# Performance work log

Hardware: AMD Instinct MI355X
Metric: run time of the kernel (lower is better)

The kernel has to match this reference:

```python
import jax, jax.numpy as jnp
import numpy as np
from jax import lax

EPS = 1e-5      # BatchNorm1d default eps
SLOPE = 0.01    # LeakyReLU default negative_slope
DN = ('NCDHW', 'OIDHW', 'NCDHW')
PAD_31 = ((1, 1), (0, 0), (1, 1))   # kernel (3,1,3), padding (1,0,1)
PAD_13 = ((0, 0), (1, 1), (1, 1))   # kernel (1,3,3), padding (0,1,1)
PAD_P = ((1, 1), (1, 1), (1, 1))    # pool kernel 3, padding 1
STRIDE_P = (2, 2, 1)                # height_pooling=False -> stride (2,2,1)


def setup_inputs() -> dict:
    key = jax.random.key(0)
    ks = jax.random.split(key, 8)
    B, Cin, Cout = 1, 32, 64
    D1, D2, D3 = 160, 160, 32
    mask = jax.random.randint(ks[0], (B, 1, D1, D2, D3), 0, 2) > 0
    x = jax.random.normal(ks[1], (B, Cin, D1, D2, D3), dtype=jnp.float32)

    def w(k, cin, cout, kd, kh, kw):
        return jax.random.normal(k, (cout, cin, kd, kh, kw), dtype=jnp.float32) * 0.05

    inp = {
        'x': x, 'mask': mask,
        'W_A1': w(ks[2], Cin, Cout, 3, 1, 3),
        'W_A2': w(ks[3], Cout, Cout, 1, 3, 3),
        'W_B1': w(ks[4], Cin, Cout, 1, 3, 3),
        'W_B2': w(ks[5], Cout, Cout, 3, 1, 3),
        'W_pool': w(ks[6], Cout, Cout, 3, 3, 3),
    }
    for name in ('A1', 'A2', 'B1', 'B2'):
        inp['g_' + name] = jnp.ones((Cout,), jnp.float32)
        inp['b_' + name] = jnp.zeros((Cout,), jnp.float32)
    return inp


def _conv(h, W, pad, stride=(1, 1, 1)):
    return lax.conv_general_dilated(h, W, stride, pad, dimension_numbers=DN)


def _lrelu(h):
    return jnp.where(h >= 0, h, SLOPE * h)


def _masked_bn(h, m, n_active, gamma, beta):
    # BatchNorm1d over the [N_active, C] sparse feature tensor:
    # per-channel stats over active voxels only (biased variance, training mode).
    mean = jnp.sum(h * m, axis=(0, 2, 3, 4)) / n_active
    mu = mean[None, :, None, None, None]
    var = jnp.sum(((h - mu) ** 2) * m, axis=(0, 2, 3, 4)) / n_active
    inv = lax.rsqrt(var + EPS)[None, :, None, None, None]
    out = (h - mu) * inv * gamma[None, :, None, None, None] + beta[None, :, None, None, None]
    return out * m  # keep inactive sites exactly zero


def reference(x, mask, W_A1, W_A2, W_B1, W_B2, W_pool,
              g_A1, b_A1, g_A2, b_A2, g_B1, b_B1, g_B2, b_B2):
    m = mask.astype(x.dtype)                      # [B,1,D1,D2,D3] active-site indicator
    n_active = jnp.sum(m)
    xs = x * m                                    # sparse input: zero at inactive voxels

    def subm(h, W, pad):
        # submanifold conv: compute only at active output sites (same site set as input)
        return _conv(h, W, pad) * m

    # branch A: conv3x1 -> LeakyReLU -> BN -> conv1x3 -> LeakyReLU -> BN
    res_A = _masked_bn(_lrelu(subm(xs, W_A1, PAD_31)), m, n_active, g_A1, b_A1)
    res_A = _masked_bn(_lrelu(subm(res_A, W_A2, PAD_13)), m, n_active, g_A2, b_A2)

    # branch B: conv1x3 -> LeakyReLU -> BN -> conv3x1 -> LeakyReLU -> BN
    res_B = _masked_bn(_lrelu(subm(xs, W_B1, PAD_13)), m, n_active, g_B1, b_B1)
    res_B = _masked_bn(_lrelu(subm(res_B, W_B2, PAD_31)), m, n_active, g_B2, b_B2)

    res_B = res_B + res_A

    # strided SparseConv3d pool: output active where any input in 3x3x3 window is active
    ones_k = jnp.ones((1, 1, 3, 3, 3), x.dtype)
    out_mask = (_conv(m, ones_k, PAD_P, STRIDE_P) > 0).astype(x.dtype)
    down = _conv(res_B, W_pool, PAD_P, STRIDE_P) * out_mask
    return (down, res_B)
```

## Files before the change

kernel.cpp:

```cpp
#include <hip/hip_runtime.h>

static constexpr int ND1=160, ND2=160, ND3=32;
static constexpr int SP  = ND1*ND2*ND3;
static constexpr int CO  = 64;
static constexpr int OD1=80, OD2=80, OD3=32;
static constexpr int OSP = OD1*OD2*OD3;
static constexpr int NSC = 64;

typedef __attribute__((ext_vector_type(8))) short  short8;
typedef __attribute__((ext_vector_type(4))) float  f32x4;

__device__ __forceinline__ float b2f(unsigned u){ return __uint_as_float(u<<16); }
__device__ __forceinline__ unsigned short f2b(float f){
    unsigned u = __float_as_uint(f);
    u += 0x7fffu + ((u>>16)&1u);
    return (unsigned short)(u>>16);
}

__global__ void k_detect(const unsigned char* __restrict__ mb, int* __restrict__ flag)
{
    __shared__ int lf;
    if (threadIdx.x == 0) lf = 0;
    __syncthreads();
    int f = 0;
    for (int i = blockIdx.x*256 + threadIdx.x; i < SP; i += gridDim.x*256) {
        unsigned char b = mb[i];
        if (b > 1) f |= 4;
        if (b != 0 && (i & 3)) f |= 1;
    }
    if (f) atomicOr(&lf, f);
    __syncthreads();
    if (threadIdx.x == 0 && lf) atomicOr(flag, lf);
}

__global__ void k_mask(const void* __restrict__ mraw, const int* __restrict__ flag,
                       float* __restrict__ m, float* __restrict__ nactN)
{
    int i = blockIdx.x*256 + threadIdx.x;
    int f = *flag;
    float v;
    if (f & 4)      v = (reinterpret_cast<const float*>(mraw)[i] != 0.f) ? 1.f : 0.f;
    else if (f & 1) v = (reinterpret_cast<const unsigned char*>(mraw)[i] != 0) ? 1.f : 0.f;
    else            v = (reinterpret_cast<const int*>(mraw)[i] != 0) ? 1.f : 0.f;
    m[i] = v;
    float s = v;
    #pragma unroll
    for (int off = 32; off > 0; off >>= 1) s += __shfl_xor(s, off);
    __shared__ float wsum[4];
    if ((threadIdx.x & 63) == 0) wsum[threadIdx.x >> 6] = s;
    __syncthreads();
    if (threadIdx.x == 0) atomicAdd(&nactN[blockIdx.x & (NSC-1)], wsum[0]+wsum[1]+wsum[2]+wsum[3]);
}

__global__ void k_finalize2(const float* __restrict__ SN0, const float* __restrict__ g0,
                            const float* __restrict__ b0, float* __restrict__ o0,
                            const float* __restrict__ SN1, const float* __restrict__ g1,
                            const float* __restrict__ b1, float* __restrict__ o1,
                            const float* __restrict__ nactN)
{
    const float* SN = blockIdx.x ? SN1 : SN0;
    const float* g  = blockIdx.x ? g1  : g0;
    const float* b  = blockIdx.x ? b1  : b0;
    float*       o  = blockIdx.x ? o1  : o0;
    int c = threadIdx.x;
    float s1 = 0.f, s2 = 0.f;
    #pragma unroll 4
    for (int k = 0; k < NSC; k++){
        s1 += SN[k*128 + c];
        s2 += SN[k*128 + 64 + c];
    }
    float nn = nactN[c];
    #pragma unroll
    for (int off = 32; off > 0; off >>= 1) nn += __shfl_xor(nn, off);
    float mean = s1 / nn;
    float var  = s2 / nn - mean*mean;
    float inv  = rsqrtf(var + 1e-5f);
    float sc   = inv * g[c];
    o[c]      = sc;
    o[64 + c] = b[c] - mean*sc;
}

__global__ void k_wprep_all(const float* __restrict__ WA1, const float* __restrict__ WA2,
                            const float* __restrict__ WB1, const float* __restrict__ WB2,
                            const float* __restrict__ WP,
                            unsigned short* __restrict__ tA1, unsigned short* __restrict__ tA2,
                            unsigned short* __restrict__ tB1, unsigned short* __restrict__ tB2,
                            unsigned short* __restrict__ tP)
{
    int i = blockIdx.x*256 + threadIdx.x;
    const float* W; unsigned short* Wt; int CIN, NT, base;
    if      (i < 18432)  { W=WA1; Wt=tA1; CIN=32; NT=9;  base=0; }
    else if (i < 55296)  { W=WA2; Wt=tA2; CIN=64; NT=9;  base=18432; }
    else if (i < 73728)  { W=WB1; Wt=tB1; CIN=32; NT=9;  base=55296; }
    else if (i < 110592) { W=WB2; Wt=tB2; CIN=64; NT=9;  base=73728; }
    else if (i < 221184) { W=WP;  Wt=tP;  CIN=64; NT=27; base=110592; }
    else return;
    int j = i - base;
    int ksub = j & 31;
    int t = j >> 5;
    int co = t & 63;
    int kc = t >> 6;
    int nch = CIN >> 5;
    int tap = kc / nch;
    int ci  = (kc - tap*nch)*32 + ksub;
    Wt[j] = f2b(W[((size_t)co*CIN + ci)*NT + tap]);
}

__global__ void k_prep_x(const float* __restrict__ x, const float* __restrict__ m,
                         unsigned short* __restrict__ xt, float* __restrict__ om)
{
    __shared__ float t[64][33];
    int sp0 = blockIdx.x*64;
    int tid = threadIdx.x;
    int c = tid>>6, s = tid&63;
    float mm = m[sp0+s];
    #pragma unroll
    for (int r=0;r<8;r++){
        int ci = c + r*4;
        t[s][ci] = x[(size_t)ci*SP + sp0 + s]*mm;
    }
    __syncthreads();
    int sp = tid>>2, c0 = (tid&3)*8;
    unsigned short o[8];
    #pragma unroll
    for (int i=0;i<8;i++) o[i] = f2b(t[sp][c0+i]);
    uint4 pk;
    pk.x = o[0] | ((unsigned)o[1]<<16);
    pk.y = o[2] | ((unsigned)o[3]<<16);
    pk.z = o[4] | ((unsigned)o[5]<<16);
    pk.w = o[6] | ((unsigned)o[7]<<16);
    *reinterpret_cast<uint4*>(xt + (size_t)(sp0+sp)*32 + c0) = pk;

    if (blockIdx.x < OSP/256){
        int i = blockIdx.x*256 + tid;
        int o3 = i & 31; int tt = i >> 5; int o2 = tt % OD2; int o1 = tt / OD2;
        float ssum = 0.f;
        for (int kd = 0; kd < 3; kd++) { int d1 = 2*o1 - 1 + kd; if ((unsigned)d1 >= ND1) continue;
          for (int kh = 0; kh < 3; kh++) { int d2 = 2*o2 - 1 + kh; if ((unsigned)d2 >= ND2) continue;
            for (int kw = 0; kw < 3; kw++) { int d3 = o3 - 1 + kw; if ((unsigned)d3 >= ND3) continue;
              ssum += m[(d1*ND2 + d2)*ND3 + d3];
            } } }
        om[i] = (ssum > 0.f) ? 1.f : 0.f;
    }
}

__global__ void k_resB(const unsigned short* __restrict__ hA, const unsigned short* __restrict__ hB,
                       const float* __restrict__ sA, const float* __restrict__ sB,
                       const float* __restrict__ m,
                       unsigned short* __restrict__ rbt, float* __restrict__ resf)
{
    __shared__ float t[64][65];
    __shared__ float ss[256];
    int tid = threadIdx.x;
    if (tid < 128){ ss[tid] = sA[tid]; ss[128+tid] = sB[tid]; }
    __syncthreads();
    int sp0 = blockIdx.x*64;
    int sp = tid>>2, c0 = (tid&3)*16;
    float mm = m[sp0+sp];
    const size_t base = (size_t)(sp0+sp)*64 + c0;
    uint4 a0 = *reinterpret_cast<const uint4*>(hA + base);
    uint4 a1 = *reinterpret_cast<const uint4*>(hA + base + 8);
    uint4 b0 = *reinterpret_cast<const uint4*>(hB + base);
    uint4 b1 = *reinterpret_cast<const uint4*>(hB + base + 8);
    unsigned ua[16] = {a0.x&0xffffu,a0.x>>16,a0.y&0xffffu,a0.y>>16,a0.z&0xffffu,a0.z>>16,a0.w&0xffffu,a0.w>>16,
                       a1.x&0xffffu,a1.x>>16,a1.y&0xffffu,a1.y>>16,a1.z&0xffffu,a1.z>>16,a1.w&0xffffu,a1.w>>16};
    unsigned ub[16] = {b0.x&0xffffu,b0.x>>16,b0.y&0xffffu,b0.y>>16,b0.z&0xffffu,b0.z>>16,b0.w&0xffffu,b0.w>>16,
                       b1.x&0xffffu,b1.x>>16,b1.y&0xffffu,b1.y>>16,b1.z&0xffffu,b1.z>>16,b1.w&0xffffu,b1.w>>16};
    unsigned short o[16];
    #pragma unroll
    for (int q=0;q<16;q++){
        int ci = c0+q;
        float v = (b2f(ua[q])*ss[ci] + ss[64+ci] + b2f(ub[q])*ss[128+ci] + ss[192+ci])*mm;
        t[sp][ci] = v;
        o[q] = f2b(v);
    }
    uint4 p0, p1;
    p0.x = o[0]|((unsigned)o[1]<<16);  p0.y = o[2]|((unsigned)o[3]<<16);
    p0.z = o[4]|((unsigned)o[5]<<16);  p0.w = o[6]|((unsigned)o[7]<<16);
    p1.x = o[8]|((unsigned)o[9]<<16);  p1.y = o[10]|((unsigned)o[11]<<16);
    p1.z = o[12]|((unsigned)o[13]<<16); p1.w = o[14]|((unsigned)o[15]<<16);
    *reinterpret_cast<uint4*>(rbt + base)     = p0;
    *reinterpret_cast<uint4*>(rbt + base + 8) = p1;
    __syncthreads();
    int ci = tid>>2, s0 = (tid&3)*16;
    #pragma unroll
    for (int kq=0;kq<4;kq++){
        float4 ov;
        ov.x = t[s0+4*kq+0][ci]; ov.y = t[s0+4*kq+1][ci];
        ov.z = t[s0+4*kq+2][ci]; ov.w = t[s0+4*kq+3][ci];
        *reinterpret_cast<float4*>(resf + (size_t)ci*SP + sp0 + s0 + 4*kq) = ov;
    }
}

template<int CIN, bool HASAFF, int KA, int KB>
__launch_bounds__(256, (CIN==32) ? 3 : 2)
__global__ void mconv_dual(const unsigned short* __restrict__ inA, const unsigned short* __restrict__ WtA,
                           const float* __restrict__ scshA, unsigned short* __restrict__ outA,
                           float* __restrict__ statsA,
                           const unsigned short* __restrict__ inB, const unsigned short* __restrict__ WtB,
                           const float* __restrict__ scshB, unsigned short* __restrict__ outB2,
                           float* __restrict__ statsB,
                           const float* __restrict__ mstage, const float* __restrict__ mout)
{
    constexpr int NCH  = CIN/32;
    constexpr int NKC  = NCH*9;
    constexpr int NR   = 10;
    constexpr int ROWB = 34*CIN*2;
    constexpr int SWZ  = (CIN==64) ? 7 : 3;
    __shared__ __align__(16) char lds[NR*ROWB];
    __shared__ float sst[128];

    const int tid = threadIdx.x;
    const int w = tid>>6, l = tid&63, g = l>>4, lj = l&15;
    const int h = w&1, rg = w>>1;

    const int bid  = blockIdx.x;
    const int hb   = (bid >= 3200) ? 1 : 0;
    const int b2   = bid - hb*3200;
    const int gi   = (b2&7)*400 + (b2>>3);
    const int kind = hb ? KB : KA;
    const unsigned short* in  = hb ? inB   : inA;
    const unsigned short* Wt  = hb ? WtB   : WtA;
    const float*        scsh  = hb ? scshB : scshA;
    unsigned short*     outb  = hb ? outB2 : outA;
    float*             statsN = hb ? statsB : statsA;

    int z  = gi % 160;
    int r0 = (gi / 160)*8;

    if (tid < 128) sst[tid] = 0.f;

    const int sd3 = tid>>3;
    const int k0  = (tid&7)*(CIN/8);

    float sc[8], sh[8];
    if (HASAFF){
        #pragma unroll
        for (int j=0;j<8;j++){ sc[j]=scsh[k0+j]; sh[j]=scsh[64+k0+j]; }
    }

    for (int i = tid; i < NR*2*(CIN/8); i += 256){
        int per = CIN/8;
        int rr = i / (2*per);
        int rem = i - rr*2*per;
        int slot = (rem >= per) ? 33 : 0;
        int kc16 = (rem >= per) ? (rem - per) : rem;
        int dst = rr*ROWB + slot*CIN*2 + kc16*16;
        dst ^= ((slot&SWZ)<<4);
        *reinterpret_cast<uint4*>(lds + dst) = make_uint4(0,0,0,0);
    }

    if (CIN==64){
        uint4 v[NR]; float mmr[NR];
        #pragma unroll
        for (int rr=0; rr<NR; rr++){
            int rw = r0 - 1 + rr;
            v[rr] = make_uint4(0,0,0,0); mmr[rr] = 0.f;
            if ((unsigned)rw < 160u){
                int vox = (kind==0) ? ((rw*ND2 + z)*ND3 + sd3)
                                    : ((z*ND2 + rw)*ND3 + sd3);
                v[rr] = *reinterpret_cast<const uint4*>(in + (size_t)vox*CIN + k0);
                if (HASAFF) mmr[rr] = mstage[vox];
            }
        }
        #pragma unroll
        for (int rr=0; rr<NR; rr++){
            uint4 vv = v[rr];
            if (HASAFF){
                float mm = mmr[rr];
                unsigned us[8] = {vv.x&0xffffu,vv.x>>16,vv.y&0xffffu,vv.y>>16,
                                  vv.z&0xffffu,vv.z>>16,vv.w&0xffffu,vv.w>>16};
                unsigned short o[8];
                #pragma unroll
                for (int j=0;j<8;j++) o[j] = f2b((b2f(us[j])*sc[j]+sh[j])*mm);
                vv.x = o[0]|((unsigned)o[1]<<16); vv.y = o[2]|((unsigned)o[3]<<16);
                vv.z = o[4]|((unsigned)o[5]<<16); vv.w = o[6]|((unsigned)o[7]<<16);
            }
            int dst = (rr*ROWB + (((sd3+1)*CIN + k0)*2)) ^ (((sd3+1)&SWZ)<<4);
            *reinterpret_cast<uint4*>(lds + dst) = vv;
        }
    } else {
        uint2 v[NR];
        #pragma unroll
        for (int rr=0; rr<NR; rr++){
            int rw = r0 - 1 + rr;
            v[rr] = make_uint2(0,0);
            if ((unsigned)rw < 160u){
                int vox = (kind==0) ? ((rw*ND2 + z)*ND3 + sd3)
                                    : ((z*ND2 + rw)*ND3 + sd3);
                v[rr] = *reinterpret_cast<const uint2*>(in + (size_t)vox*CIN + k0);
            }
        }
        #pragma unroll
        for (int rr=0; rr<NR; rr++){
            int dst = (rr*ROWB + (((sd3+1)*CIN + k0)*2)) ^ (((sd3+1)&SWZ)<<4);
            *reinterpret_cast<uint2*>(lds + dst) = v[rr];
        }
    }

    short8 pa[NKC][2];
    {
        const unsigned short* wb = Wt + (size_t)(h*32)*32 + lj*32 + g*8;
        #pragma unroll
        for (int kc=0; kc<NKC; kc++){
            pa[kc][0] = *reinterpret_cast<const short8*>(wb + (size_t)kc*2048);
            pa[kc][1] = *reinterpret_cast<const short8*>(wb + (size_t)kc*2048 + 512);
        }
    }

    int tb[8], ovox[8];
    float mm[8];
    #pragma unroll
    for (int t=0;t<8;t++){
        int rowb = rg*4 + (t>>1);
        int o3   = (t&1)*16 + lj;
        tb[t] = rowb*ROWB + ((o3*CIN + g*8)*2);
        int o2r = r0 + rowb;
        ovox[t] = (kind==0) ? ((o2r*ND2 + z)*ND3 + o3)
                            : ((z*ND2 + o2r)*ND3 + o3);
        mm[t] = mout[ovox[t]];
    }
    int swz[3];
    #pragma unroll
    for (int kw=0;kw<3;kw++) swz[kw] = ((lj+kw)&SWZ)<<4;

    __syncthreads();

    f32x4 acc[2][8];
    #pragma unroll
    for (int c=0;c<2;c++)
        #pragma unroll
        for (int t=0;t<8;t++)
            #pragma unroll
            for (int q=0;q<4;q++) acc[c][t][q] = 0.f;

    #pragma unroll
    for (int ch=0; ch<NCH; ch++){
        #pragma unroll
        for (int tap=0; tap<9; tap++){
            const int kd = tap/3, kw = tap - kd*3;
            const int kc = tap*NCH + ch;
            const int tapoff = kd*ROWB + (kw*CIN + ch*32)*2;
            #pragma unroll
            for (int t=0;t<8;t++){
                int off = (tb[t] + tapoff) ^ swz[kw];
                short8 bv = *reinterpret_cast<const short8*>(lds + off);
                acc[0][t] = __builtin_amdgcn_mfma_f32_16x16x32_bf16(pa[kc][0], bv, acc[0][t], 0,0,0);
                acc[1][t] = __builtin_amdgcn_mfma_f32_16x16x32_bf16(pa[kc][1], bv, acc[1][t], 0,0,0);
            }
        }
    }

    #pragma unroll
    for (int c=0;c<2;c++){
        const int ct = h*2 + c;
        float s1[4] = {0.f,0.f,0.f,0.f};
        float s2[4] = {0.f,0.f,0.f,0.f};
        #pragma unroll
        for (int t=0;t<8;t++){
            float v[4];
            #pragma unroll
            for (int r=0;r<4;r++){
                float xv = acc[c][t][r]*mm[t];
                xv = (xv >= 0.f) ? xv : 0.01f*xv;
                v[r] = xv; s1[r] += xv; s2[r] += xv*xv;
            }
            unsigned lo = f2b(v[0]) | ((unsigned)f2b(v[1])<<16);
            unsigned hi = f2b(v[2]) | ((unsigned)f2b(v[3])<<16);
            *reinterpret_cast<uint2*>(outb + (size_t)ovox[t]*64 + ct*16 + g*4) = make_uint2(lo,hi);
        }
        #pragma unroll
        for (int r=0;r<4;r++){
            float a = s1[r], b = s2[r];
            a += __shfl_xor(a,1); b += __shfl_xor(b,1);
            a += __shfl_xor(a,2); b += __shfl_xor(b,2);
            a += __shfl_xor(a,4); b += __shfl_xor(b,4);
            a += __shfl_xor(a,8); b += __shfl_xor(b,8);
            if (lj == 0){
                atomicAdd(&sst[ct*16 + g*4 + r], a);
                atomicAdd(&sst[64 + ct*16 + g*4 + r], b);
            }
        }
    }
    __syncthreads();
    if (tid < 128){
        float* sg = statsN + (size_t)(blockIdx.x & (NSC-1))*128;
        atomicAdd(&sg[tid], sst[tid]);
    }
}

__launch_bounds__(256, 2)
__global__ void mpool5(const unsigned short* __restrict__ in,
                       const unsigned short* __restrict__ Wt,
                       const float* __restrict__ mout,
                       float* __restrict__ outf)
{
    constexpr int SLOTB = 80;
    constexpr int ROWB  = 34*SLOTB;
    extern __shared__ __align__(16) char lds[];

    const int tid = threadIdx.x;
    const int w = tid>>6, l = tid&63, g = l>>4, lj = l&15;
    const int h = w&1, rg = w>>1;

    int gi = (blockIdx.x & 7)*(gridDim.x>>3) + (blockIdx.x>>3);
    int z  = gi % OD1;
    int r0 = (gi / OD1)*4;

    const int sd3 = tid>>3;
    const int kq  = tid&7;

    for (int i = tid; i < 27*2*4; i += 256){
        int row = i >> 3, rem = i & 7;
        int slot = (rem >= 4) ? 33 : 0;
        int c16 = rem & 3;
        *reinterpret_cast<uint4*>(lds + row*ROWB + slot*SLOTB + c16*16) = make_uint4(0,0,0,0);
    }

    int ovx[4];
    float om[4];
    #pragma unroll
    for (int t=0;t<4;t++){
        int row = rg*2 + (t>>1);
        int o3  = (t&1)*16 + lj;
        ovx[t] = (z*OD2 + (r0 + row))*OD3 + o3;
        om[t]  = mout[ovx[t]];
    }

    f32x4 acc[2][4];
    #pragma unroll
    for (int c=0;c<2;c++)
        #pragma unroll
        for (int t=0;t<4;t++)
            #pragma unroll
            for (int q=0;q<4;q++) acc[c][t][q] = 0.f;

    const unsigned short* wbase = Wt + (size_t)(h*32)*32 + lj*32 + g*8;

    #pragma unroll 1
    for (int ph=0; ph<2; ph++){
        uint2 v[27];
        #pragma unroll
        for (int i=0;i<27;i++){
            const int kd = i/9, rr = i - (i/9)*9;
            int d1 = 2*z - 1 + kd;
            int d2 = 2*r0 - 1 + rr;
            v[i] = make_uint2(0,0);
            if ((unsigned)d1 < (unsigned)ND1 && (unsigned)d2 < (unsigned)ND2){
                int vox = (d1*ND2 + d2)*ND3 + sd3;
                v[i] = *reinterpret_cast<const uint2*>(in + (size_t)vox*64 + ph*32 + kq*4);
            }
        }
        __syncthreads();
        #pragma unroll
        for (int i=0;i<27;i++){
            *reinterpret_cast<uint2*>(lds + i*ROWB + (sd3+1)*SLOTB + kq*8) = v[i];
        }
        __syncthreads();

        #pragma unroll
        for (int kd=0; kd<3; kd++){
            short8 pa[9][2];
            #pragma unroll
            for (int tap=0; tap<9; tap++){
                const int kc = (kd*9 + tap)*2 + ph;
                pa[tap][0] = *reinterpret_cast<const short8*>(wbase + (size_t)kc*2048);
                pa[tap][1] = *reinterpret_cast<const short8*>(wbase + (size_t)kc*2048 + 512);
            }
            #pragma unroll
            for (int tap=0; tap<9; tap++){
                const int kh = tap/3, kw = tap - (tap/3)*3;
                #pragma unroll
                for (int t=0;t<4;t++){
                    const int rr = 2*(rg*2 + (t>>1)) + kh;
                    const int slot = (t&1)*16 + lj + kw;
                    const char* bp = lds + (kd*9 + rr)*ROWB + slot*SLOTB + g*16;
                    short8 bv = *reinterpret_cast<const short8*>(bp);
                    acc[0][t] = __builtin_amdgcn_mfma_f32_16x16x32_bf16(pa[tap][0], bv, acc[0][t], 0,0,0);
                    acc[1][t] = __builtin_amdgcn_mfma_f32_16x16x32_bf16(pa[tap][1], bv, acc[1][t], 0,0,0);
                }
            }
        }
    }

    __syncthreads();
    float* olds = (float*)lds;
    #pragma unroll
    for (int c=0;c<2;c++){
        const int ct = h*2 + c;
        #pragma unroll
        for (int t=0;t<4;t++){
            int row = rg*2 + (t>>1);
            int o3  = (t&1)*16 + lj;
            #pragma unroll
            for (int r=0;r<4;r++){
                int co = ct*16 + g*4 + r;
                olds[co*128 + row*32 + o3] = acc[c][t][r]*om[t];
            }
        }
    }
    __syncthreads();
    const size_t obase = (size_t)(z*OD2 + r0)*OD3;
    #pragma unroll
    for (int i=0;i<8;i++){
        int idx = i*256 + tid;
        int co  = idx >> 5;
        int q   = idx & 31;
        uint4 v = *reinterpret_cast<uint4*>(reinterpret_cast<char*>(olds) + co*512 + q*16);
        *reinterpret_cast<uint4*>(outf + (size_t)co*OSP + obase + q*4) = v;
    }
}

extern "C" void kernel_launch(void* const* d_in, const int* in_sizes, int n_in,
                              void* d_out, int out_size, void* d_ws, size_t ws_size,
                              hipStream_t stream)
{
    const float* x      = (const float*)d_in[0];
    const void*  mraw   = d_in[1];
    const float* W_A1   = (const float*)d_in[2];
    const float* W_A2   = (const float*)d_in[3];
    const float* W_B1   = (const float*)d_in[4];
    const float* W_B2   = (const float*)d_in[5];
    const float* W_pool = (const float*)d_in[6];
    const float* g_A1 = (const float*)d_in[7],  *b_A1 = (const float*)d_in[8];
    const float* g_A2 = (const float*)d_in[9],  *b_A2 = (const float*)d_in[10];
    const float* g_B1 = (const float*)d_in[11], *b_B1 = (const float*)d_in[12];
    const float* g_B2 = (const float*)d_in[13], *b_B2 = (const float*)d_in[14];

    char* p = (char*)d_ws;
    float* m     = (float*)p; p += (size_t)SP*4;
    float* omask = (float*)p; p += (size_t)OSP*4;
    float* statsN= (float*)p; p += 4*NSC*128*4;
    float* scsh  = (float*)p; p += 4*128*4;
    float* nactN = (float*)p; p += NSC*4;
    int*   flag  = (int*)p;   p += 4;
    p += 252;
    unsigned short* WtA1 = (unsigned short*)p; p += 288*64*2;
    unsigned short* WtA2 = (unsigned short*)p; p += 576*64*2;
    unsigned short* WtB1 = (unsigned short*)p; p += 288*64*2;
    unsigned short* WtB2 = (unsigned short*)p; p += 576*64*2;
    unsigned short* WtP  = (unsigned short*)p; p += 1728*64*2;
    unsigned short* X = (unsigned short*)p; p += (size_t)SP*32*2;
    unsigned short* P = (unsigned short*)p; p += (size_t)SP*64*2;
    unsigned short* Q = (unsigned short*)p; p += (size_t)SP*64*2;
    unsigned short* R = (unsigned short*)p; p += (size_t)SP*64*2;
    unsigned short* S = (unsigned short*)p; p += (size_t)SP*64*2;

    float* down = (float*)d_out;
    float* resf = down + (size_t)CO*OSP;

    const int shmP = 27*34*80;
    hipFuncSetAttribute((const void*)&mpool5, hipFuncAttributeMaxDynamicSharedMemorySize, shmP);

    hipMemsetAsync(statsN, 0, (4*NSC*128 + 4*128 + NSC)*4 + 4, stream);
    k_detect<<<256, 256, 0, stream>>>((const unsigned char*)mraw, flag);
    k_mask<<<SP/256, 256, 0, stream>>>(mraw, flag, m, nactN);
    k_wprep_all<<<864, 256, 0, stream>>>(W_A1, W_A2, W_B1, W_B2, W_pool,
                                         WtA1, WtA2, WtB1, WtB2, WtP);
    k_prep_x<<<SP/64, 256, 0, stream>>>(x, m, X, omask);

    float* SA1 = statsN + 0*NSC*128;
    float* SA2 = statsN + 1*NSC*128;
    float* SB1 = statsN + 2*NSC*128;
    float* SB2 = statsN + 3*NSC*128;

    mconv_dual<32,false,0,1><<<6400, 256, 0, stream>>>(
        X, WtA1, nullptr, P, SA1,
        X, WtB1, nullptr, Q, SB1, nullptr, m);
    k_finalize2<<<2, 64, 0, stream>>>(SA1, g_A1, b_A1, scsh + 0,
                                      SB1, g_B1, b_B1, scsh + 256, nactN);
    mconv_dual<64,true,1,0><<<6400, 256, 0, stream>>>(
        P, WtA2, scsh + 0,   R, SA2,
        Q, WtB2, scsh + 256, S, SB2, m, m);
    k_finalize2<<<2, 64, 0, stream>>>(SA2, g_A2, b_A2, scsh + 128,
                                      SB2, g_B2, b_B2, scsh + 384, nactN);
    k_resB<<<SP/64, 256, 0, stream>>>(R, S, scsh + 128, scsh + 384, m, Q, resf);
    mpool5<<<1600, 256, shmP, stream>>>(Q, WtP, omask, down);
}
```

Baseline: 638.7 us.

## Cut register pressure in dual conv and stage output through LDS

Weight fragments are now loaded per input-channel chunk inside a non-unrolled loop instead of being held all at once in registers. The output mask and voxel index computation is deferred until after the MMA loop. Launch bounds are raised to three blocks for both channel widths. The bf16 conv output is written into a padded LDS staging buffer and then copied to global memory as coalesced 16-byte stores, replacing the scattered 8-byte stores. The goal is higher occupancy and better write coalescing, at the cost of an extra barrier, more LDS per block, and weight reloads per chunk.

```diff
diff --git a/kernel.cpp b/kernel.cpp
--- a/kernel.cpp
+++ b/kernel.cpp
@@ -193,7 +193,7 @@
 }
 
 template<int CIN, bool HASAFF, int KA, int KB>
-__launch_bounds__(256, (CIN==32) ? 3 : 2)
+__launch_bounds__(256, 3)
 __global__ void mconv_dual(const unsigned short* __restrict__ inA, const unsigned short* __restrict__ WtA,
                            const float* __restrict__ scshA, unsigned short* __restrict__ outA,
                            float* __restrict__ statsA,
@@ -203,11 +203,12 @@
                            const float* __restrict__ mstage, const float* __restrict__ mout)
 {
     constexpr int NCH  = CIN/32;
-    constexpr int NKC  = NCH*9;
     constexpr int NR   = 10;
     constexpr int ROWB = 34*CIN*2;
     constexpr int SWZ  = (CIN==64) ? 7 : 3;
-    __shared__ __align__(16) char lds[NR*ROWB];
+    constexpr int OBST = 144;
+    constexpr int LDSZ = (NR*ROWB > 256*OBST) ? NR*ROWB : 256*OBST;
+    __shared__ __align__(16) char lds[LDSZ];
     __shared__ float sst[128];
 
     const int tid = threadIdx.x;
@@ -298,27 +299,12 @@
         }
     }
 
-    short8 pa[NKC][2];
-    {
-        const unsigned short* wb = Wt + (size_t)(h*32)*32 + lj*32 + g*8;
-        #pragma unroll
-        for (int kc=0; kc<NKC; kc++){
-            pa[kc][0] = *reinterpret_cast<const short8*>(wb + (size_t)kc*2048);
-            pa[kc][1] = *reinterpret_cast<const short8*>(wb + (size_t)kc*2048 + 512);
-        }
-    }
-
-    int tb[8], ovox[8];
-    float mm[8];
+    int tb[8];
     #pragma unroll
     for (int t=0;t<8;t++){
         int rowb = rg*4 + (t>>1);
         int o3   = (t&1)*16 + lj;
         tb[t] = rowb*ROWB + ((o3*CIN + g*8)*2);
-        int o2r = r0 + rowb;
-        ovox[t] = (kind==0) ? ((o2r*ND2 + z)*ND3 + o3)
-                            : ((z*ND2 + o2r)*ND3 + o3);
-        mm[t] = mout[ovox[t]];
     }
     int swz[3];
     #pragma unroll
@@ -334,23 +320,43 @@
             #pragma unroll
             for (int q=0;q<4;q++) acc[c][t][q] = 0.f;
 
-    #pragma unroll
+    const unsigned short* wb = Wt + (size_t)(h*32)*32 + lj*32 + g*8;
+
+    #pragma unroll 1
     for (int ch=0; ch<NCH; ch++){
+        short8 pa[9][2];
+        #pragma unroll
+        for (int tap=0; tap<9; tap++){
+            const int kc = tap*NCH + ch;
+            pa[tap][0] = *reinterpret_cast<const short8*>(wb + (size_t)kc*2048);
+            pa[tap][1] = *reinterpret_cast<const short8*>(wb + (size_t)kc*2048 + 512);
+        }
         #pragma unroll
         for (int tap=0; tap<9; tap++){
             const int kd = tap/3, kw = tap - kd*3;
-            const int kc = tap*NCH + ch;
             const int tapoff = kd*ROWB + (kw*CIN + ch*32)*2;
             #pragma unroll
             for (int t=0;t<8;t++){
                 int off = (tb[t] + tapoff) ^ swz[kw];
                 short8 bv = *reinterpret_cast<const short8*>(lds + off);
-                acc[0][t] = __builtin_amdgcn_mfma_f32_16x16x32_bf16(pa[kc][0], bv, acc[0][t], 0,0,0);
-                acc[1][t] = __builtin_amdgcn_mfma_f32_16x16x32_bf16(pa[kc][1], bv, acc[1][t], 0,0,0);
-            }
-        }
-    }
-
+                acc[0][t] = __builtin_amdgcn_mfma_f32_16x16x32_bf16(pa[tap][0], bv, acc[0][t], 0,0,0);
+                acc[1][t] = __builtin_amdgcn_mfma_f32_16x16x32_bf16(pa[tap][1], bv, acc[1][t], 0,0,0);
+            }
+        }
+    }
+
+    __syncthreads();
+
+    float mmv[8];
+    #pragma unroll
+    for (int t=0;t<8;t++){
+        int rowb = rg*4 + (t>>1);
+        int o3   = (t&1)*16 + lj;
+        int o2r  = r0 + rowb;
+        int ovox = (kind==0) ? ((o2r*ND2 + z)*ND3 + o3)
+                             : ((z*ND2 + o2r)*ND3 + o3);
+        mmv[t] = mout[ovox];
+    }
     #pragma unroll
     for (int c=0;c<2;c++){
         const int ct = h*2 + c;
@@ -358,16 +364,19 @@
         float s2[4] = {0.f,0.f,0.f,0.f};
         #pragma unroll
         for (int t=0;t<8;t++){
+            int rowb = rg*4 + (t>>1);
+            int o3   = (t&1)*16 + lj;
+            int vloc = rowb*32 + o3;
             float v[4];
             #pragma unroll
             for (int r=0;r<4;r++){
-                float xv = acc[c][t][r]*mm[t];
+                float xv = acc[c][t][r]*mmv[t];
                 xv = (xv >= 0.f) ? xv : 0.01f*xv;
                 v[r] = xv; s1[r] += xv; s2[r] += xv*xv;
             }
             unsigned lo = f2b(v[0]) | ((unsigned)f2b(v[1])<<16);
             unsigned hi = f2b(v[2]) | ((unsigned)f2b(v[3])<<16);
-            *reinterpret_cast<uint2*>(outb + (size_t)ovox[t]*64 + ct*16 + g*4) = make_uint2(lo,hi);
+            *reinterpret_cast<uint2*>(lds + vloc*OBST + (ct*16 + g*4)*2) = make_uint2(lo,hi);
         }
         #pragma unroll
         for (int r=0;r<4;r++){
@@ -383,6 +392,18 @@
         }
     }
     __syncthreads();
+    #pragma unroll
+    for (int i=0;i<8;i++){
+        int idx = i*256 + tid;
+        int vloc = idx >> 3;
+        int q    = idx & 7;
+        int row  = vloc >> 5;
+        int o3g  = vloc & 31;
+        int gvox = (kind==0) ? (((r0+row)*ND2 + z)*ND3 + o3g)
+                             : ((z*ND2 + (r0+row))*ND3 + o3g);
+        uint4 v = *reinterpret_cast<uint4*>(lds + vloc*OBST + q*16);
+        *reinterpret_cast<uint4*>(outb + (size_t)gvox*64 + q*8) = v;
+    }
     if (tid < 128){
         float* sg = statsN + (size_t)(blockIdx.x & (NSC-1))*128;
         atomicAdd(&sg[tid], sst[tid]);
```

Measured after the change: 582.3 us. 1.1x faster.
